# Kernel optimization log

Measured on AMD Instinct MI355X. Metric: run time of the kernel, lower is better.

## Reference

```python
import jax, jax.numpy as jnp
import numpy as np

K = 16          # nodes_num
BN_EPS = 1e-5


def _bn_conv_relu(x, w, gamma, beta, mean, var):
    # 1x1 conv on [N,K,C] node features == matmul, then eval-mode BN + ReLU
    y = jnp.einsum('nkc,oc->nko', x, w)                      # [N,K,256]
    y = (y - mean) * jax.lax.rsqrt(var + BN_EPS) * gamma + beta
    return jax.nn.relu(y)


def _lnorm(r, c):
    # Symmetric-normalized affinity from node pixel coordinates.
    # A_ij = 1/(1+||p_i-p_j||), self-loops A_ii=1, Lnorm = D^-1/2 A D^-1/2
    p = jnp.stack([r, c], axis=-1).astype(jnp.float32)        # [N,K,2]
    diff = p[:, :, None, :] - p[:, None, :, :]
    dist = jnp.sqrt(jnp.sum(diff * diff, axis=-1))            # [N,K,K]
    A = 1.0 / (1.0 + dist)
    dinv = jax.lax.rsqrt(jnp.sum(A, axis=-1))                 # [N,K]
    return A * dinv[:, :, None] * dinv[:, None, :]


def setup_inputs() -> dict:
    key = jax.random.key(0)
    ks = jax.random.split(key, 12)
    N, C, W, H = 128, 1024, 14, 14
    O = 256
    inp = {
        'fpam_output': jax.random.normal(ks[0], (N, C, W, H), jnp.float32),
        'resnet_output': jax.random.normal(ks[1], (N, 2048), jnp.float32),
        'w_max': jax.random.normal(ks[2], (O, C), jnp.float32) * 0.02,
        'g_max': 1.0 + 0.1 * jax.random.normal(ks[3], (O,), jnp.float32),
        'b_max': 0.1 * jax.random.normal(ks[4], (O,), jnp.float32),
        'm_max': 0.1 * jax.random.normal(ks[5], (O,), jnp.float32),
        'v_max': jax.random.uniform(ks[6], (O,), jnp.float32, 0.5, 1.5),
        'w_med': jax.random.normal(ks[7], (O, C), jnp.float32) * 0.02,
        'g_med': 1.0 + 0.1 * jax.random.normal(ks[8], (O,), jnp.float32),
        'b_med': 0.1 * jax.random.normal(ks[9], (O,), jnp.float32),
        'm_med': 0.1 * jax.random.normal(ks[10], (O,), jnp.float32),
        'v_med': jax.random.uniform(ks[11], (O,), jnp.float32, 0.5, 1.5),
    }
    return inp


def reference(fpam_output, resnet_output, w_max, g_max, b_max, m_max, v_max,
              w_med, g_med, b_med, m_med, v_med):
    N, C, W, H = fpam_output.shape
    HW = W * H
    # channel-sum saliency, sort descending
    fre = jnp.sum(fpam_output, axis=1).reshape(N, HW)         # [N,HW]
    idx = jnp.argsort(-fre, axis=1)
    maxK = idx[:, :K]
    mstart = HW // 2 - K // 2 - 1
    medK = idx[:, mstart:mstart + K]
    scene = jnp.concatenate([maxK, medK], axis=1)             # [N,2K]
    rows = scene // H
    cols = scene % H
    # batched gather replacing the per-pixel python loop
    flat = fpam_output.reshape(N, C, HW)
    nodes = jnp.take_along_axis(flat, scene[:, None, :], axis=2)  # [N,C,2K]
    nodes = jnp.transpose(nodes, (0, 2, 1))                   # [N,2K,C]
    x_max = _bn_conv_relu(nodes[:, :K], w_max, g_max, b_max, m_max, v_max)
    x_med = _bn_conv_relu(nodes[:, K:], w_med, g_med, b_med, m_med, v_med)
    Ltop = _lnorm(rows[:, :K], cols[:, :K])
    Lmed = _lnorm(rows[:, K:], cols[:, K:])
    max_graph = jnp.einsum('nij,njc->nic', Ltop, x_max).reshape(N, -1)
    med_graph = jnp.einsum('nij,njc->nic', Lmed, x_med).reshape(N, -1)
    return (max_graph, med_graph, rows, cols)
```

## Files before the change

### kernel.cpp

```cpp
#include <hip/hip_runtime.h>

#define NB 128
#define CC 1024
#define HWP 196
#define HH 14
#define OO 256

typedef unsigned short ushort_t;
typedef __attribute__((ext_vector_type(8))) short short8;
typedef __attribute__((ext_vector_type(4))) float float4v;

__device__ __forceinline__ ushort_t f2bf(float v) {
  union { float f; unsigned int u; } c; c.f = v;
  unsigned int u = c.u;
  unsigned int r = (u + 0x7FFFu + ((u >> 16) & 1u)) >> 16;
  return (ushort_t)r;
}

__global__ __launch_bounds__(256) void k_prep(const float* __restrict__ x,
                                              const float* __restrict__ wmax,
                                              const float* __restrict__ wmed,
                                              float* __restrict__ partial,
                                              ushort_t* __restrict__ wb) {
  const int b = blockIdx.x, t = threadIdx.x;
  if (b >= 1024) {
    int idx = (b - 1024) * 256 + t;
    int z = idx >> 18;
    int r = idx & (OO * CC - 1);
    const float* w = z ? wmed : wmax;
    wb[idx] = f2bf(w[r]);
    return;
  }
  const int n = b >> 3, cg = b & 7;
  const int p = t;
  if (p >= HWP) return;
  const float* base = x + ((size_t)n * CC + (size_t)cg * 128) * HWP + p;
  float s = 0.f;
  #pragma unroll 16
  for (int c = 0; c < 128; ++c) s += base[(size_t)c * HWP];
  partial[((size_t)n * 8 + cg) * HWP + p] = s;
}

__global__ __launch_bounds__(256) void k_main(
    const float* __restrict__ x, const float* __restrict__ partial,
    const ushort_t* __restrict__ wb,
    const float* __restrict__ g_max, const float* __restrict__ b_max,
    const float* __restrict__ m_max, const float* __restrict__ v_max,
    const float* __restrict__ g_med, const float* __restrict__ b_med,
    const float* __restrict__ m_med, const float* __restrict__ v_med,
    float* __restrict__ out) {
  constexpr int AP = 1032;
  __shared__ ushort_t A_sh[16 * AP];
  __shared__ float fre[HWP];
  __shared__ int sc[32];
  __shared__ float Lsh[16][17];
  __shared__ float dinv[16];
  __shared__ float y_sh[16][257];

  const int n = blockIdx.x;
  const int z = blockIdx.y;
  const int t = threadIdx.x;

  if (t < HWP) {
    float s = 0.f;
    #pragma unroll
    for (int g = 0; g < 8; ++g) s += partial[((size_t)n * 8 + g) * HWP + t];
    fre[t] = s;
  }
  __syncthreads();
  if (t < HWP) {
    float v = fre[t];
    int rank = 0;
    #pragma unroll 4
    for (int q = 0; q < HWP; ++q) {
      float u = fre[q];
      rank += ((u > v) || (u == v && q < t)) ? 1 : 0;
    }
    if (rank < 16) sc[rank] = t;
    else if (rank >= 89 && rank < 105) sc[rank - 73] = t;
  }
  __syncthreads();

  if (z == 0 && t < 32) {
    int p = sc[t];
    out[2 * NB * 4096 + n * 32 + t] = (float)(p / HH);
    out[2 * NB * 4096 + NB * 32 + n * 32 + t] = (float)(p % HH);
  }

  {
    const int j = t & 15;
    const int kg = t >> 4;
    const int sj = sc[z * 16 + j];
    const float* xb = x + (size_t)n * (CC * HWP) + sj;
    ushort_t* arow = &A_sh[j * AP];
    #pragma unroll 8
    for (int u = 0; u < 64; ++u) {
      int k = kg * 64 + u;
      arow[k] = f2bf(xb[(size_t)k * HWP]);
    }
  }
  {
    const int i = t >> 4, j = t & 15;
    int pi = sc[z * 16 + i], pj = sc[z * 16 + j];
    float dr = (float)(pi / HH - pj / HH);
    float dc = (float)(pi % HH - pj % HH);
    Lsh[i][j] = 1.0f / (1.0f + sqrtf(dr * dr + dc * dc));
  }
  __syncthreads();
  if (t < 16) {
    float s = 0.f;
    #pragma unroll
    for (int j = 0; j < 16; ++j) s += Lsh[t][j];
    dinv[t] = rsqrtf(s);
  }

  const int w = t >> 6;
  const int l = t & 63;
  const int m = l & 15;
  const int quad = l >> 4;

  const ushort_t* Arow = &A_sh[m * AP + quad * 8];
  const ushort_t* B0 = wb + (size_t)z * (OO * CC) + (size_t)(w * 64 + m) * CC + quad * 8;

  float4v acc0 = {0.f, 0.f, 0.f, 0.f};
  float4v acc1 = acc0, acc2 = acc0, acc3 = acc0;

  __syncthreads();

  #pragma unroll 4
  for (int k0 = 0; k0 < CC; k0 += 32) {
    short8 a  = *reinterpret_cast<const short8*>(Arow + k0);
    short8 b0 = *reinterpret_cast<const short8*>(B0 + k0);
    short8 b1 = *reinterpret_cast<const short8*>(B0 + 16 * CC + k0);
    short8 b2 = *reinterpret_cast<const short8*>(B0 + 32 * CC + k0);
    short8 b3 = *reinterpret_cast<const short8*>(B0 + 48 * CC + k0);
    acc0 = __builtin_amdgcn_mfma_f32_16x16x32_bf16(a, b0, acc0, 0, 0, 0);
    acc1 = __builtin_amdgcn_mfma_f32_16x16x32_bf16(a, b1, acc1, 0, 0, 0);
    acc2 = __builtin_amdgcn_mfma_f32_16x16x32_bf16(a, b2, acc2, 0, 0, 0);
    acc3 = __builtin_amdgcn_mfma_f32_16x16x32_bf16(a, b3, acc3, 0, 0, 0);
  }

  const float* gp = z ? g_med : g_max;
  const float* bp = z ? b_med : b_max;
  const float* mp = z ? m_med : m_max;
  const float* vp = z ? v_med : v_max;

  #pragma unroll
  for (int tt = 0; tt < 4; ++tt) {
    float4v av = (tt == 0) ? acc0 : (tt == 1) ? acc1 : (tt == 2) ? acc2 : acc3;
    int o = w * 64 + tt * 16 + m;
    float scale = gp[o] * rsqrtf(vp[o] + 1e-5f);
    float shift = bp[o] - mp[o] * scale;
    #pragma unroll
    for (int r = 0; r < 4; ++r) {
      int j = quad * 4 + r;
      float y = av[r] * scale + shift;
      y = fmaxf(y, 0.f);
      y_sh[j][o] = y * dinv[j];
    }
  }
  __syncthreads();

  float yp[16];
  #pragma unroll
  for (int j = 0; j < 16; ++j) yp[j] = y_sh[j][t];
  float* ob = out + (size_t)z * (NB * 4096) + (size_t)n * 4096 + t;
  #pragma unroll
  for (int i = 0; i < 16; ++i) {
    float s = 0.f;
    #pragma unroll
    for (int j = 0; j < 16; ++j) s = fmaf(Lsh[i][j], yp[j], s);
    ob[(size_t)i * OO] = s * dinv[i];
  }
}

extern "C" void kernel_launch(void* const* d_in, const int* in_sizes, int n_in,
                              void* d_out, int out_size, void* d_ws, size_t ws_size,
                              hipStream_t stream) {
  const float* x     = (const float*)d_in[0];
  const float* w_max = (const float*)d_in[2];
  const float* g_max = (const float*)d_in[3];
  const float* b_max = (const float*)d_in[4];
  const float* m_max = (const float*)d_in[5];
  const float* v_max = (const float*)d_in[6];
  const float* w_med = (const float*)d_in[7];
  const float* g_med = (const float*)d_in[8];
  const float* b_med = (const float*)d_in[9];
  const float* m_med = (const float*)d_in[10];
  const float* v_med = (const float*)d_in[11];
  float* out = (float*)d_out;

  float* ws_f = (float*)d_ws;
  float* partial  = ws_f;
  ushort_t* wb    = (ushort_t*)(ws_f + 200704);

  k_prep<<<dim3(1024 + 2048), 256, 0, stream>>>(x, w_max, w_med, partial, wb);
  k_main<<<dim3(NB, 2), 256, 0, stream>>>(x, partial, wb,
                                          g_max, b_max, m_max, v_max,
                                          g_med, b_med, m_med, v_med, out);
}
```

Before: 211.4 us.

## Vectorize channel-sum prep and widen main kernel to 512 threads

The channel-sum prep now reads float4 vectors, with each 64-lane wavefront handling one (batch, channel-group) unit, so it needs a quarter as many blocks. The main kernel doubles its block to 512 threads: each wave covers 32 output channels with two MFMA accumulators instead of 64 with four, the node gather is split over twice as many threads, and the final Laplacian product is split across two row halves. The aim is more memory parallelism and latency hiding in the gather and GEMM phases, at the cost of larger blocks and an extra launch-bounds constraint that may limit occupancy.

```diff
diff --git a/kernel.cpp b/kernel.cpp
--- a/kernel.cpp
+++ b/kernel.cpp
@@ -23,25 +23,29 @@
                                               float* __restrict__ partial,
                                               ushort_t* __restrict__ wb) {
   const int b = blockIdx.x, t = threadIdx.x;
-  if (b >= 1024) {
-    int idx = (b - 1024) * 256 + t;
+  if (b >= 256) {
+    int idx = (b - 256) * 256 + t;
     int z = idx >> 18;
     int r = idx & (OO * CC - 1);
     const float* w = z ? wmed : wmax;
     wb[idx] = f2bf(w[r]);
     return;
   }
-  const int n = b >> 3, cg = b & 7;
-  const int p = t;
-  if (p >= HWP) return;
-  const float* base = x + ((size_t)n * CC + (size_t)cg * 128) * HWP + p;
-  float s = 0.f;
+  const int unit = b * 4 + (t >> 6);
+  const int lane = t & 63;
+  if (lane >= 49) return;
+  const int n = unit >> 3, cg = unit & 7;
+  const float4* base = (const float4*)(x + ((size_t)n * CC + (size_t)cg * 128) * HWP);
+  float4 s = {0.f, 0.f, 0.f, 0.f};
   #pragma unroll 16
-  for (int c = 0; c < 128; ++c) s += base[(size_t)c * HWP];
-  partial[((size_t)n * 8 + cg) * HWP + p] = s;
-}
-
-__global__ __launch_bounds__(256) void k_main(
+  for (int c = 0; c < 128; ++c) {
+    float4 v = base[c * 49 + lane];
+    s.x += v.x; s.y += v.y; s.z += v.z; s.w += v.w;
+  }
+  ((float4*)(partial + ((size_t)n * 8 + cg) * HWP))[lane] = s;
+}
+
+__global__ __launch_bounds__(512, 2) void k_main(
     const float* __restrict__ x, const float* __restrict__ partial,
     const ushort_t* __restrict__ wb,
     const float* __restrict__ g_max, const float* __restrict__ b_max,
@@ -50,7 +54,7 @@
     const float* __restrict__ m_med, const float* __restrict__ v_med,
     float* __restrict__ out) {
   constexpr int AP = 1032;
-  __shared__ ushort_t A_sh[16 * AP];
+  __shared__ alignas(16) ushort_t A_sh[16 * AP];
   __shared__ float fre[HWP];
   __shared__ int sc[32];
   __shared__ float Lsh[16][17];
@@ -89,17 +93,16 @@
 
   {
     const int j = t & 15;
-    const int kg = t >> 4;
+    const int g = t >> 4;
     const int sj = sc[z * 16 + j];
-    const float* xb = x + (size_t)n * (CC * HWP) + sj;
-    ushort_t* arow = &A_sh[j * AP];
-    #pragma unroll 8
-    for (int u = 0; u < 64; ++u) {
-      int k = kg * 64 + u;
-      arow[k] = f2bf(xb[(size_t)k * HWP]);
-    }
-  }
-  {
+    const float* xb = x + (size_t)n * (CC * HWP) + (size_t)g * 32 * HWP + sj;
+    ushort_t* arow = &A_sh[j * AP + g * 32];
+    #pragma unroll 16
+    for (int u = 0; u < 32; ++u) {
+      arow[u] = f2bf(xb[(size_t)u * HWP]);
+    }
+  }
+  if (t < 256) {
     const int i = t >> 4, j = t & 15;
     int pi = sc[z * 16 + i], pj = sc[z * 16 + j];
     float dr = (float)(pi / HH - pj / HH);
@@ -120,10 +123,10 @@
   const int quad = l >> 4;
 
   const ushort_t* Arow = &A_sh[m * AP + quad * 8];
-  const ushort_t* B0 = wb + (size_t)z * (OO * CC) + (size_t)(w * 64 + m) * CC + quad * 8;
+  const ushort_t* B0 = wb + (size_t)z * (OO * CC) + (size_t)(w * 32 + m) * CC + quad * 8;
 
   float4v acc0 = {0.f, 0.f, 0.f, 0.f};
-  float4v acc1 = acc0, acc2 = acc0, acc3 = acc0;
+  float4v acc1 = acc0;
 
   __syncthreads();
 
@@ -132,12 +135,8 @@
     short8 a  = *reinterpret_cast<const short8*>(Arow + k0);
     short8 b0 = *reinterpret_cast<const short8*>(B0 + k0);
     short8 b1 = *reinterpret_cast<const short8*>(B0 + 16 * CC + k0);
-    short8 b2 = *reinterpret_cast<const short8*>(B0 + 32 * CC + k0);
-    short8 b3 = *reinterpret_cast<const short8*>(B0 + 48 * CC + k0);
     acc0 = __builtin_amdgcn_mfma_f32_16x16x32_bf16(a, b0, acc0, 0, 0, 0);
     acc1 = __builtin_amdgcn_mfma_f32_16x16x32_bf16(a, b1, acc1, 0, 0, 0);
-    acc2 = __builtin_amdgcn_mfma_f32_16x16x32_bf16(a, b2, acc2, 0, 0, 0);
-    acc3 = __builtin_amdgcn_mfma_f32_16x16x32_bf16(a, b3, acc3, 0, 0, 0);
   }
 
   const float* gp = z ? g_med : g_max;
@@ -146,9 +145,9 @@
   const float* vp = z ? v_med : v_max;
 
   #pragma unroll
-  for (int tt = 0; tt < 4; ++tt) {
-    float4v av = (tt == 0) ? acc0 : (tt == 1) ? acc1 : (tt == 2) ? acc2 : acc3;
-    int o = w * 64 + tt * 16 + m;
+  for (int tt = 0; tt < 2; ++tt) {
+    float4v av = tt ? acc1 : acc0;
+    int o = w * 32 + tt * 16 + m;
     float scale = gp[o] * rsqrtf(vp[o] + 1e-5f);
     float shift = bp[o] - mp[o] * scale;
     #pragma unroll
@@ -161,16 +160,21 @@
   }
   __syncthreads();
 
-  float yp[16];
-  #pragma unroll
-  for (int j = 0; j < 16; ++j) yp[j] = y_sh[j][t];
-  float* ob = out + (size_t)z * (NB * 4096) + (size_t)n * 4096 + t;
-  #pragma unroll
-  for (int i = 0; i < 16; ++i) {
-    float s = 0.f;
-    #pragma unroll
-    for (int j = 0; j < 16; ++j) s = fmaf(Lsh[i][j], yp[j], s);
-    ob[(size_t)i * OO] = s * dinv[i];
+  {
+    const int o = t & 255;
+    const int ih = (t >> 8) * 8;
+    float yp[16];
+    #pragma unroll
+    for (int j = 0; j < 16; ++j) yp[j] = y_sh[j][o];
+    float* ob = out + (size_t)z * (NB * 4096) + (size_t)n * 4096 + o;
+    #pragma unroll
+    for (int i2 = 0; i2 < 8; ++i2) {
+      const int i = ih + i2;
+      float s = 0.f;
+      #pragma unroll
+      for (int j = 0; j < 16; ++j) s = fmaf(Lsh[i][j], yp[j], s);
+      ob[(size_t)i * OO] = s * dinv[i];
+    }
   }
 }
 
@@ -194,8 +198,8 @@
   float* partial  = ws_f;
   ushort_t* wb    = (ushort_t*)(ws_f + 200704);
 
-  k_prep<<<dim3(1024 + 2048), 256, 0, stream>>>(x, w_max, w_med, partial, wb);
-  k_main<<<dim3(NB, 2), 256, 0, stream>>>(x, partial, wb,
+  k_prep<<<dim3(256 + 2048), 256, 0, stream>>>(x, w_max, w_med, partial, wb);
+  k_main<<<dim3(NB, 2), 512, 0, stream>>>(x, partial, wb,
                                           g_max, b_max, m_max, v_max,
                                           g_med, b_med, m_med, v_med, out);
 }
```

New measurement: 208.3 us. About the same (-1.5%).
